# Optimization experiments

Hardware: AMD Instinct MI355X
Metric: run time of the kernel (lower is better)

Reference implementation:

```python
import jax, jax.numpy as jnp
import numpy as np

B, D, N, E = 4, 128, 16384, 65536  # batch, feature_dim, n_junctions, 2*n_lines
EPS = 1e-5  # BatchNorm eps


def setup_inputs() -> dict:
    key = jax.random.key(0)
    ks = jax.random.split(key, 8)
    s = lambda k, shape: jax.random.normal(k, shape, dtype=jnp.float32)
    return {
        "ldesc0": s(ks[0], (B, D, N)),
        "ldesc1": s(ks[1], (B, D, N)),
        "line_enc0": s(ks[2], (B, D, E)),
        "line_enc1": s(ks[3], (B, D, E)),
        "lines_junc_idx0": jax.random.randint(ks[4], (B, E), 0, N),
        "lines_junc_idx1": jax.random.randint(ks[5], (B, E), 0, N),
        # MLP([3D, 2D, D]) params: conv1x1 -> BN -> ReLU -> conv1x1
        "w1": s(ks[6], (2 * D, 3 * D)) * 0.05,
        "b1": jnp.zeros((2 * D,), jnp.float32),
        "bn_gamma": jnp.ones((2 * D,), jnp.float32),
        "bn_beta": jnp.zeros((2 * D,), jnp.float32),
        "bn_mean": jnp.zeros((2 * D,), jnp.float32),
        "bn_var": jnp.ones((2 * D,), jnp.float32),
        "w2": s(ks[7], (D, 2 * D)) * 0.05,
        "b2": jnp.zeros((D,), jnp.float32),
    }


def _mlp(x, w1, b1, g, beta, mu, var, w2, b2):
    # x: [B, 3D, E] -> [B, D, E]; BN in inference mode with running stats
    h = jnp.einsum('oi,bie->boe', w1, x) + b1[None, :, None]
    scale = g / jnp.sqrt(var + EPS)
    h = h * scale[None, :, None] + (beta - mu * scale)[None, :, None]
    h = jax.nn.relu(h)
    return jnp.einsum('oi,bie->boe', w2, h) + b2[None, :, None]


def _endpoint_update(ldesc, line_enc, idx, params):
    # gather endpoint descriptors: [B, D, E]
    line_desc = jax.vmap(lambda x, i: x[:, i])(ldesc, idx)
    b, d, e = line_desc.shape
    # swap the two endpoints of each line (flip along the size-2 axis)
    flipped = line_desc.reshape(b, d, e // 2, 2)[..., ::-1].reshape(b, d, e)
    message = jnp.concatenate([line_desc, flipped, line_enc], axis=1)  # [B, 3D, E]
    return _mlp(message, *params)


def _scatter_mean(src, idx, n):
    # src: [B, D, E], idx: [B, E] -> mean-reduced [B, D, n]; empty slots stay 0
    def one(s, i):
        sums = jax.ops.segment_sum(s.T, i, num_segments=n)                    # [n, D]
        cnt = jax.ops.segment_sum(jnp.ones(s.shape[1], s.dtype), i, num_segments=n)
        return (sums / jnp.maximum(cnt, 1.0)[:, None]).T                      # [D, n]
    return jax.vmap(one)(src, idx)


def reference(ldesc0, ldesc1, line_enc0, line_enc1, lines_junc_idx0, lines_junc_idx1,
              w1, b1, bn_gamma, bn_beta, bn_mean, bn_var, w2, b2):
    params = (w1, b1, bn_gamma, bn_beta, bn_mean, bn_var, w2, b2)
    up0 = _endpoint_update(ldesc0, line_enc0, lines_junc_idx0, params)
    up1 = _endpoint_update(ldesc1, line_enc1, lines_junc_idx1, params)
    n = ldesc0.shape[2]
    out0 = ldesc0 + _scatter_mean(up0, lines_junc_idx0, n)
    out1 = ldesc1 + _scatter_mean(up1, lines_junc_idx1, n)
    return (out0, out1)
```

## Files before the change

### kernel.cpp

```cpp
#include <hip/hip_runtime.h>
#include <hip/hip_bf16.h>
#include <stdint.h>

#define Bb 4
#define Dd 128
#define Nn 16384
#define Ee 65536
#define NTB 16

typedef __attribute__((ext_vector_type(4))) float f32x4;
typedef __attribute__((ext_vector_type(8))) short s16x8;

__device__ __forceinline__ unsigned short f2bf(float f) {
  union { float f; unsigned int u; } v; v.f = f;
  unsigned int r = v.u + 0x7fffu + ((v.u >> 16) & 1u);
  return (unsigned short)(r >> 16);
}

__device__ __forceinline__ unsigned int cvtpk(float lo, float hi) {
  unsigned int r;
  asm volatile("v_cvt_pk_bf16_f32 %0, %1, %2" : "=v"(r) : "v"(lo), "v"(hi));
  return r;
}

__global__ void prep_weights(const float* __restrict__ w1, const float* __restrict__ b1,
                             const float* __restrict__ g, const float* __restrict__ beta,
                             const float* __restrict__ mu, const float* __restrict__ var,
                             const float* __restrict__ w2,
                             unsigned short* __restrict__ W1s, unsigned short* __restrict__ W2s,
                             float* __restrict__ c1) {
  int i = blockIdx.x * 256 + threadIdx.x;
  if (i < 256 * 384) {
    int o = i / 384;
    float scale = g[o] * rsqrtf(var[o] + 1e-5f);
    W1s[i] = f2bf(w1[i] * scale);
  }
  if (i < 128 * 256) W2s[i] = f2bf(w2[i]);
  if (i < 256) {
    float scale = g[i] * rsqrtf(var[i] + 1e-5f);
    c1[i] = b1[i] * scale + beta[i] - mu[i] * scale;
  }
}

__global__ void transpose_ldesc(const float* __restrict__ l0, const float* __restrict__ l1,
                                unsigned short* __restrict__ dst, int side0) {
  __shared__ float tile[32][33];
  int z = blockIdx.z;
  int gs = side0 + (z >> 2), b = z & 3;
  const float* src = (gs ? l1 : l0) + (size_t)b * Dd * Nn;
  unsigned short* d = dst + (size_t)z * Nn * Dd;
  int n0 = blockIdx.x * 32;
  int d0 = blockIdx.y * 32;
  int tx = threadIdx.x, ty = threadIdx.y;
#pragma unroll
  for (int i = 0; i < 4; ++i)
    tile[ty + i * 8][tx] = src[(size_t)(d0 + ty + i * 8) * Nn + n0 + tx];
  __syncthreads();
#pragma unroll
  for (int i = 0; i < 4; ++i) {
    int r = ty + i * 8;
    d[(size_t)(n0 + r) * Dd + d0 + tx] = f2bf(tile[tx][r]);
  }
}

__global__ void hist_kernel(const int* __restrict__ idx0, const int* __restrict__ idx1,
                            int* __restrict__ hist) {
  int i = blockIdx.x * 256 + threadIdx.x;
  int sb = i >> 16;
  int e = i & 65535;
  const int* jx = (sb >= 4) ? idx1 : idx0;
  int n = jx[(size_t)(sb & 3) * Ee + e];
  atomicAdd(&hist[sb * Nn + n], 1);
}

__global__ __launch_bounds__(1024) void scan_kernel(const int* __restrict__ hist,
                                                    int* __restrict__ offs,
                                                    int* __restrict__ cursor) {
  __shared__ int part[1024];
  int sb = blockIdx.x, t = threadIdx.x;
  const int* h = hist + sb * Nn;
  int base = t * 16;
  int v[16];
  int local = 0;
#pragma unroll
  for (int i = 0; i < 16; ++i) { v[i] = local; local += h[base + i]; }
  part[t] = local;
  __syncthreads();
  for (int d = 1; d < 1024; d <<= 1) {
    int y = (t >= d) ? part[t - d] : 0;
    __syncthreads();
    part[t] += y;
    __syncthreads();
  }
  int excl = part[t] - local;
#pragma unroll
  for (int i = 0; i < 16; ++i) {
    int o = excl + v[i];
    offs[sb * Nn + base + i] = o;
    cursor[sb * Nn + base + i] = o;
  }
}

__global__ void fill_kernel(const int* __restrict__ idx0, const int* __restrict__ idx1,
                            int* __restrict__ cursor, int* __restrict__ elist) {
  int i = blockIdx.x * 256 + threadIdx.x;
  int sb = i >> 16;
  int e = i & 65535;
  const int* jx = (sb >= 4) ? idx1 : idx0;
  int n = jx[(size_t)(sb & 3) * Ee + e];
  int pos = atomicAdd(&cursor[sb * Nn + n], 1);
  elist[(size_t)sb * Ee + pos] = e;
}

#define STAGE_DESC(ti, buf)                                                     \
  do {                                                                          \
    int e0s_ = (tile0 + (ti)) * 64;                                             \
    unsigned char* xb_ = sm + (buf) * 32768;                                    \
    int cA_ = w * 8 + (lane >> 4);                                              \
    int cB_ = cA_ + 4;                                                          \
    int uA_ = (lane & 15) ^ (cA_ & 7);                                          \
    int uB_ = (lane & 15) ^ (cB_ & 7);                                          \
    int iA_ = jxB[e0s_ + cA_];                                                  \
    int iB_ = jxB[e0s_ + cB_];                                                  \
    __builtin_amdgcn_global_load_lds(                                           \
        (const __attribute__((address_space(1))) void*)(ldB + ((size_t)iA_) * 128 + uA_ * 8), \
        (__attribute__((address_space(3))) void*)(xb_ + (w * 8) * 256), 16, 0, 0); \
    __builtin_amdgcn_global_load_lds(                                           \
        (const __attribute__((address_space(1))) void*)(ldB + ((size_t)iB_) * 128 + uB_ * 8), \
        (__attribute__((address_space(3))) void*)(xb_ + (w * 8 + 4) * 256), 16, 0, 0); \
  } while (0)

#define ENC_LOAD(ti)                                                            \
  do {                                                                          \
    int e0s_ = (tile0 + (ti)) * 64;                                             \
    const float* es_ = enF + (size_t)(oct * 8) * Ee + e0s_ + ep * 2;            \
    _Pragma("unroll") for (int r = 0; r < 8; ++r)                               \
      ereg[r] = *(const float2*)(es_ + (size_t)r * Ee);                         \
  } while (0)

#define ENC_WRITE(buf)                                                          \
  do {                                                                          \
    unsigned char* xb_ = sm + (buf) * 32768;                                    \
    _Pragma("unroll") for (int j = 0; j < 2; ++j) {                             \
      int e_ = ep * 2 + j;                                                      \
      uint4 pk_;                                                                \
      pk_.x = cvtpk(j ? ereg[0].y : ereg[0].x, j ? ereg[1].y : ereg[1].x);      \
      pk_.y = cvtpk(j ? ereg[2].y : ereg[2].x, j ? ereg[3].y : ereg[3].x);      \
      pk_.z = cvtpk(j ? ereg[4].y : ereg[4].x, j ? ereg[5].y : ereg[5].x);      \
      pk_.w = cvtpk(j ? ereg[6].y : ereg[6].x, j ? ereg[7].y : ereg[7].x);      \
      *(uint4*)(xb_ + 16384 + e_ * 256 + ((oct ^ (e_ & 7)) << 4)) = pk_;        \
    }                                                                           \
  } while (0)

__global__ __launch_bounds__(512, 2) void fused_mlp_ws(
    const unsigned short* __restrict__ ldescT,
    const float* __restrict__ enc0, const float* __restrict__ enc1,
    const int* __restrict__ idx0, const int* __restrict__ idx1, int side0,
    const unsigned short* __restrict__ W1s, const unsigned short* __restrict__ W2s,
    const float* __restrict__ c1, const float* __restrict__ b2,
    unsigned short* __restrict__ U) {
  __shared__ __align__(16) unsigned char sm[65536];

  const int t = threadIdx.x;
  const int w = t >> 6;
  const int lane = t & 63;
  const int lr = t & 15;
  const int lk = (t & 63) >> 4;
  const int oct = t >> 5;
  const int ep = t & 31;
  const int ls = blockIdx.x >> 8;
  const int gs = side0 + ls;
  const int bB = (blockIdx.x >> 6) & 3;
  const int tile0 = (blockIdx.x & 63) * NTB;

  const int* jxB = (gs ? idx1 : idx0) + (size_t)bB * Ee;
  const unsigned short* ldB = ldescT + ((size_t)(ls * Bb + bB)) * Nn * 128;
  const float* enF = (gs ? enc1 : enc0) + (size_t)bB * Dd * Ee;
  unsigned short* UB = U + ((size_t)(ls * Bb + bB)) * Ee * 128;

  s16x8 w1f[2][12];
#pragma unroll
  for (int rt = 0; rt < 2; ++rt)
#pragma unroll
    for (int ks = 0; ks < 12; ++ks)
      w1f[rt][ks] = *(const s16x8*)&W1s[(size_t)(w * 32 + rt * 16 + lr) * 384 + ks * 32 + lk * 8];
  s16x8 w2f[8];
#pragma unroll
  for (int ks = 0; ks < 8; ++ks)
    w2f[ks] = *(const s16x8*)&W2s[(size_t)(w * 16 + lr) * 256 + ks * 32 + lk * 8];
  float c1v[2][4], b2v[4];
#pragma unroll
  for (int rt = 0; rt < 2; ++rt)
#pragma unroll
    for (int r = 0; r < 4; ++r) c1v[rt][r] = c1[w * 32 + rt * 16 + lk * 4 + r];
#pragma unroll
  for (int r = 0; r < 4; ++r) b2v[r] = b2[w * 16 + lk * 4 + r];

  float2 ereg[8];

  STAGE_DESC(0, 0);
  STAGE_DESC(1, 1);
  ENC_LOAD(0);
  asm volatile("s_waitcnt vmcnt(0)" ::: "memory");
  ENC_WRITE(0);
  ENC_LOAD(1);
  asm volatile("s_waitcnt vmcnt(0)" ::: "memory");
  ENC_WRITE(1);
  asm volatile("s_waitcnt lgkmcnt(0)" ::: "memory");
  __builtin_amdgcn_s_barrier();
  __builtin_amdgcn_sched_barrier(0);

#pragma unroll 1
  for (int i = 0; i < NTB; ++i) {
    const int p = i & 1;
    unsigned short* xb = (unsigned short*)(sm + p * 32768);
    unsigned short* hb = xb;
    const int e0c = (tile0 + i) * 64;

    f32x4 acc[2][4] = {};
    __builtin_amdgcn_s_setprio(1);
#pragma unroll
    for (int ks = 0; ks < 12; ++ks) {
      s16x8 bf[4];
#pragma unroll
      for (int ct = 0; ct < 4; ++ct) {
        int c = ct * 16 + lr;
        int off;
        if (ks < 4)      { off = c * 128 + (((ks * 4 + lk) ^ (c & 7)) * 8); }
        else if (ks < 8) { int c2 = c ^ 1; off = c2 * 128 + ((((ks - 4) * 4 + lk) ^ (c2 & 7)) * 8); }
        else             { off = 8192 + c * 128 + ((((ks - 8) * 4 + lk) ^ (c & 7)) * 8); }
        bf[ct] = *(const s16x8*)&xb[off];
      }
#pragma unroll
      for (int rt = 0; rt < 2; ++rt)
#pragma unroll
        for (int ct = 0; ct < 4; ++ct)
          acc[rt][ct] = __builtin_amdgcn_mfma_f32_16x16x32_bf16(w1f[rt][ks], bf[ct], acc[rt][ct], 0, 0, 0);
    }
    __builtin_amdgcn_s_setprio(0);
    asm volatile("s_waitcnt lgkmcnt(0)" ::: "memory");
    __builtin_amdgcn_s_barrier();
    __builtin_amdgcn_sched_barrier(0);

#pragma unroll
    for (int rt = 0; rt < 2; ++rt) {
      int rowbase = w * 32 + rt * 16 + lk * 4;
      int unitr = rowbase >> 3, inner = rowbase & 7;
#pragma unroll
      for (int ct = 0; ct < 4; ++ct) {
        int col = ct * 16 + lr;
        float v0 = fmaxf(acc[rt][ct][0] + c1v[rt][0], 0.f);
        float v1 = fmaxf(acc[rt][ct][1] + c1v[rt][1], 0.f);
        float v2 = fmaxf(acc[rt][ct][2] + c1v[rt][2], 0.f);
        float v3 = fmaxf(acc[rt][ct][3] + c1v[rt][3], 0.f);
        uint2 pk;
        pk.x = cvtpk(v0, v1);
        pk.y = cvtpk(v2, v3);
        *(uint2*)&hb[col * 256 + ((unitr ^ (col & 7)) * 8) + inner] = pk;
      }
    }

    if (i + 2 < NTB) ENC_LOAD(i + 2);

    asm volatile("s_waitcnt lgkmcnt(0)" ::: "memory");
    __builtin_amdgcn_s_barrier();
    __builtin_amdgcn_sched_barrier(0);

    f32x4 acc2[4] = {};
    __builtin_amdgcn_s_setprio(1);
#pragma unroll
    for (int ks = 0; ks < 8; ++ks) {
      s16x8 bf[4];
#pragma unroll
      for (int ct = 0; ct < 4; ++ct) {
        int c = ct * 16 + lr;
        bf[ct] = *(const s16x8*)&hb[c * 256 + (((ks * 4 + lk) ^ (c & 7)) * 8)];
      }
#pragma unroll
      for (int ct = 0; ct < 4; ++ct)
        acc2[ct] = __builtin_amdgcn_mfma_f32_16x16x32_bf16(w2f[ks], bf[ct], acc2[ct], 0, 0, 0);
    }
    __builtin_amdgcn_s_setprio(0);

#pragma unroll
    for (int ct = 0; ct < 4; ++ct) {
      int col = ct * 16 + lr;
      uint2 pk;
      pk.x = cvtpk(acc2[ct][0] + b2v[0], acc2[ct][1] + b2v[1]);
      pk.y = cvtpk(acc2[ct][2] + b2v[2], acc2[ct][3] + b2v[3]);
      *(uint2*)&UB[(((size_t)(e0c + col)) << 7) + w * 16 + lk * 4] = pk;
    }

    asm volatile("s_waitcnt lgkmcnt(0)" ::: "memory");
    __builtin_amdgcn_s_barrier();
    __builtin_amdgcn_sched_barrier(0);

    if (i + 2 < NTB) {
      asm volatile("s_waitcnt vmcnt(0)" ::: "memory");
      ENC_WRITE(p);
      STAGE_DESC(i + 2, p);
    }

    if (i + 1 < NTB) {
      if (i + 2 >= NTB)
        asm volatile("s_waitcnt vmcnt(0)" ::: "memory");
      asm volatile("s_waitcnt lgkmcnt(0)" ::: "memory");
      __builtin_amdgcn_s_barrier();
      __builtin_amdgcn_sched_barrier(0);
    }
  }
}

__global__ __launch_bounds__(256) void scatter_finalize(
    const unsigned short* __restrict__ U, const int* __restrict__ elist,
    const int* __restrict__ offs, const float* __restrict__ l0,
    const float* __restrict__ l1, float* __restrict__ out, int side0) {
  __shared__ float lsum[64][129];
  const int ls = blockIdx.z;
  const int gs = side0 + ls;
  const int b = blockIdx.y;
  const int n0 = blockIdx.x * 64;
  const int t = threadIdx.x;
  const int w = t >> 6, lane = t & 63;
  const unsigned int* Uu = (const unsigned int*)(U + ((size_t)(ls * Bb + b)) * Ee * 128);
  const int* elist_s = elist + ((size_t)(gs * Bb + b)) * Ee;
  const int* offs_s = offs + ((size_t)(gs * Bb + b)) * Nn;
  const float* l = (gs ? l1 : l0) + (size_t)b * Dd * Nn;
  float* o = out + ((size_t)(gs * Bb + b)) * Dd * Nn;

#pragma unroll 1
  for (int q = 0; q < 16; ++q) {
    int jj = w * 16 + q;
    int n = n0 + jj;
    int s = offs_s[n];
    int e_end = (n == Nn - 1) ? Ee : offs_s[n + 1];
    float s0 = 0.f, s1 = 0.f;
    for (int k = s; k < e_end; ++k) {
      int e = elist_s[k];
      unsigned int p = Uu[(((size_t)e) << 6) + lane];
      union { unsigned int u; float f; } lo, hi;
      lo.u = p << 16;
      hi.u = p & 0xffff0000u;
      s0 += lo.f;
      s1 += hi.f;
    }
    float inv = (e_end > s) ? 1.0f / (float)(e_end - s) : 0.0f;
    lsum[jj][lane * 2] = s0 * inv;
    lsum[jj][lane * 2 + 1] = s1 * inv;
  }
  __syncthreads();

  int nloc = t & 63;
  int dbase = (t >> 6) * 32;
#pragma unroll
  for (int i = 0; i < 32; ++i) {
    int d = dbase + i;
    size_t off2 = (size_t)d * Nn + n0 + nloc;
    o[off2] = l[off2] + lsum[nloc][d];
  }
}

extern "C" void kernel_launch(void* const* d_in, const int* in_sizes, int n_in,
                              void* d_out, int out_size, void* d_ws, size_t ws_size,
                              hipStream_t stream) {
  const float* ldesc0 = (const float*)d_in[0];
  const float* ldesc1 = (const float*)d_in[1];
  const float* enc0   = (const float*)d_in[2];
  const float* enc1   = (const float*)d_in[3];
  const int*   idx0   = (const int*)d_in[4];
  const int*   idx1   = (const int*)d_in[5];
  const float* w1     = (const float*)d_in[6];
  const float* b1     = (const float*)d_in[7];
  const float* g      = (const float*)d_in[8];
  const float* beta   = (const float*)d_in[9];
  const float* mu     = (const float*)d_in[10];
  const float* var    = (const float*)d_in[11];
  const float* w2     = (const float*)d_in[12];
  const float* b2     = (const float*)d_in[13];
  float* out = (float*)d_out;

  char* ws = (char*)d_ws;
  size_t off = 0;
  unsigned short* W1s = (unsigned short*)(ws + off); off += 256 * 384 * 2;
  unsigned short* W2s = (unsigned short*)(ws + off); off += 128 * 256 * 2;
  float* c1   = (float*)(ws + off); off += 256 * 4;
  int* hist   = (int*)(ws + off); off += (size_t)8 * Nn * 4;
  int* offs   = (int*)(ws + off); off += (size_t)8 * Nn * 4;
  int* cursor = (int*)(ws + off); off += (size_t)8 * Nn * 4;
  int* elist  = (int*)(ws + off); off += (size_t)8 * Ee * 4;
  size_t small_end = off;

  const size_t tside = (size_t)Bb * Nn * Dd * 2;
  const size_t bigside = (size_t)Bb * Ee * Dd * 2;
  size_t need_full = small_end + 2 * tside + 2 * bigside;
  const bool full = (ws_size >= need_full);
  const int sides_buf = full ? 2 : 1;

  unsigned short* t = (unsigned short*)(ws + off); off += tside * sides_buf;
  unsigned short* U = (unsigned short*)(ws + off); off += bigside * sides_buf;

  hipMemsetAsync(hist, 0, (size_t)8 * Nn * 4, stream);
  prep_weights<<<384, 256, 0, stream>>>(w1, b1, g, beta, mu, var, w2, W1s, W2s, c1);
  hist_kernel<<<2048, 256, 0, stream>>>(idx0, idx1, hist);
  scan_kernel<<<8, 1024, 0, stream>>>(hist, offs, cursor);
  fill_kernel<<<2048, 256, 0, stream>>>(idx0, idx1, cursor, elist);

  if (full) {
    transpose_ldesc<<<dim3(Nn / 32, Dd / 32, 8), dim3(32, 8), 0, stream>>>(
        ldesc0, ldesc1, t, 0);
    fused_mlp_ws<<<512, 512, 0, stream>>>(t, enc0, enc1, idx0, idx1, 0,
                                          W1s, W2s, c1, b2, U);
    scatter_finalize<<<dim3(Nn / 64, Bb, 2), 256, 0, stream>>>(
        U, elist, offs, ldesc0, ldesc1, out, 0);
  } else {
    for (int side = 0; side < 2; ++side) {
      transpose_ldesc<<<dim3(Nn / 32, Dd / 32, 4), dim3(32, 8), 0, stream>>>(
          ldesc0, ldesc1, t, side);
      fused_mlp_ws<<<256, 512, 0, stream>>>(t, enc0, enc1, idx0, idx1, side,
                                            W1s, W2s, c1, b2, U);
      scatter_finalize<<<dim3(Nn / 64, Bb, 1), 256, 0, stream>>>(
          U, elist, offs, ldesc0, ldesc1, out, side);
    }
  }
}
```

Before: 460.5 us.

## Write MLP outputs in junction-sorted order and deepen encoder prefetch pipeline

fill_kernel now stores each edge's sorted position (perm), and the fused MLP writes each edge's output row directly at that position. The scatter kernel can then read U contiguously per junction without the elist indirection. The MLP kernel also gets a separate 32KB LDS buffer for the hidden activations, so one barrier per tile can be dropped and the encoder loads can run three tiles ahead with partial vmcnt waits. In exchange, LDS per block grows to 96KB, which may lower occupancy below the 2 blocks per CU that the launch bounds target, and the U stores become scattered rows.

```diff
diff --git a/kernel.cpp b/kernel.cpp
--- a/kernel.cpp
+++ b/kernel.cpp
@@ -102,14 +102,14 @@
 }
 
 __global__ void fill_kernel(const int* __restrict__ idx0, const int* __restrict__ idx1,
-                            int* __restrict__ cursor, int* __restrict__ elist) {
+                            int* __restrict__ cursor, int* __restrict__ perm) {
   int i = blockIdx.x * 256 + threadIdx.x;
   int sb = i >> 16;
   int e = i & 65535;
   const int* jx = (sb >= 4) ? idx1 : idx0;
   int n = jx[(size_t)(sb & 3) * Ee + e];
   int pos = atomicAdd(&cursor[sb * Nn + n], 1);
-  elist[(size_t)sb * Ee + pos] = e;
+  perm[(size_t)sb * Ee + e] = pos;
 }
 
 #define STAGE_DESC(ti, buf)                                                     \
@@ -156,10 +156,11 @@
     const unsigned short* __restrict__ ldescT,
     const float* __restrict__ enc0, const float* __restrict__ enc1,
     const int* __restrict__ idx0, const int* __restrict__ idx1, int side0,
+    const int* __restrict__ perm,
     const unsigned short* __restrict__ W1s, const unsigned short* __restrict__ W2s,
     const float* __restrict__ c1, const float* __restrict__ b2,
     unsigned short* __restrict__ U) {
-  __shared__ __align__(16) unsigned char sm[65536];
+  __shared__ __align__(16) unsigned char sm[98304];
 
   const int t = threadIdx.x;
   const int w = t >> 6;
@@ -174,6 +175,7 @@
   const int tile0 = (blockIdx.x & 63) * NTB;
 
   const int* jxB = (gs ? idx1 : idx0) + (size_t)bB * Ee;
+  const int* permB = perm + ((size_t)(gs * Bb + bB)) * Ee;
   const unsigned short* ldB = ldescT + ((size_t)(ls * Bb + bB)) * Nn * 128;
   const float* enF = (gs ? enc1 : enc0) + (size_t)bB * Dd * Ee;
   unsigned short* UB = U + ((size_t)(ls * Bb + bB)) * Ee * 128;
@@ -197,6 +199,7 @@
   for (int r = 0; r < 4; ++r) b2v[r] = b2[w * 16 + lk * 4 + r];
 
   float2 ereg[8];
+  unsigned short* hb = (unsigned short*)(sm + 65536);
 
   STAGE_DESC(0, 0);
   STAGE_DESC(1, 1);
@@ -206,6 +209,7 @@
   ENC_LOAD(1);
   asm volatile("s_waitcnt vmcnt(0)" ::: "memory");
   ENC_WRITE(1);
+  if (2 < NTB) ENC_LOAD(2);
   asm volatile("s_waitcnt lgkmcnt(0)" ::: "memory");
   __builtin_amdgcn_s_barrier();
   __builtin_amdgcn_sched_barrier(0);
@@ -213,9 +217,12 @@
 #pragma unroll 1
   for (int i = 0; i < NTB; ++i) {
     const int p = i & 1;
-    unsigned short* xb = (unsigned short*)(sm + p * 32768);
-    unsigned short* hb = xb;
+    const unsigned short* xb = (const unsigned short*)(sm + p * 32768);
     const int e0c = (tile0 + i) * 64;
+
+    int prow[4];
+#pragma unroll
+    for (int ct = 0; ct < 4; ++ct) prow[ct] = permB[e0c + ct * 16 + lr];
 
     f32x4 acc[2][4] = {};
     __builtin_amdgcn_s_setprio(1);
@@ -238,9 +245,6 @@
           acc[rt][ct] = __builtin_amdgcn_mfma_f32_16x16x32_bf16(w1f[rt][ks], bf[ct], acc[rt][ct], 0, 0, 0);
     }
     __builtin_amdgcn_s_setprio(0);
-    asm volatile("s_waitcnt lgkmcnt(0)" ::: "memory");
-    __builtin_amdgcn_s_barrier();
-    __builtin_amdgcn_sched_barrier(0);
 
 #pragma unroll
     for (int rt = 0; rt < 2; ++rt) {
@@ -259,12 +263,20 @@
         *(uint2*)&hb[col * 256 + ((unitr ^ (col & 7)) * 8) + inner] = pk;
       }
     }
-
-    if (i + 2 < NTB) ENC_LOAD(i + 2);
-
     asm volatile("s_waitcnt lgkmcnt(0)" ::: "memory");
     __builtin_amdgcn_s_barrier();
     __builtin_amdgcn_sched_barrier(0);
+
+    if (i == 0) {
+      asm volatile("s_waitcnt vmcnt(4)" ::: "memory");
+    } else {
+      asm volatile("s_waitcnt vmcnt(8)" ::: "memory");
+    }
+    if (i + 2 < NTB) {
+      ENC_WRITE(p);
+      STAGE_DESC(i + 2, p);
+    }
+    if (i + 3 < NTB) ENC_LOAD(i + 3);
 
     f32x4 acc2[4] = {};
     __builtin_amdgcn_s_setprio(1);
@@ -284,26 +296,13 @@
 
 #pragma unroll
     for (int ct = 0; ct < 4; ++ct) {
-      int col = ct * 16 + lr;
       uint2 pk;
       pk.x = cvtpk(acc2[ct][0] + b2v[0], acc2[ct][1] + b2v[1]);
       pk.y = cvtpk(acc2[ct][2] + b2v[2], acc2[ct][3] + b2v[3]);
-      *(uint2*)&UB[(((size_t)(e0c + col)) << 7) + w * 16 + lk * 4] = pk;
-    }
-
-    asm volatile("s_waitcnt lgkmcnt(0)" ::: "memory");
-    __builtin_amdgcn_s_barrier();
-    __builtin_amdgcn_sched_barrier(0);
-
-    if (i + 2 < NTB) {
-      asm volatile("s_waitcnt vmcnt(0)" ::: "memory");
-      ENC_WRITE(p);
-      STAGE_DESC(i + 2, p);
+      *(uint2*)&UB[(((size_t)prow[ct]) << 7) + w * 16 + lk * 4] = pk;
     }
 
     if (i + 1 < NTB) {
-      if (i + 2 >= NTB)
-        asm volatile("s_waitcnt vmcnt(0)" ::: "memory");
       asm volatile("s_waitcnt lgkmcnt(0)" ::: "memory");
       __builtin_amdgcn_s_barrier();
       __builtin_amdgcn_sched_barrier(0);
@@ -312,7 +311,7 @@
 }
 
 __global__ __launch_bounds__(256) void scatter_finalize(
-    const unsigned short* __restrict__ U, const int* __restrict__ elist,
+    const unsigned short* __restrict__ U,
     const int* __restrict__ offs, const float* __restrict__ l0,
     const float* __restrict__ l1, float* __restrict__ out, int side0) {
   __shared__ float lsum[64][129];
@@ -323,7 +322,6 @@
   const int t = threadIdx.x;
   const int w = t >> 6, lane = t & 63;
   const unsigned int* Uu = (const unsigned int*)(U + ((size_t)(ls * Bb + b)) * Ee * 128);
-  const int* elist_s = elist + ((size_t)(gs * Bb + b)) * Ee;
   const int* offs_s = offs + ((size_t)(gs * Bb + b)) * Nn;
   const float* l = (gs ? l1 : l0) + (size_t)b * Dd * Nn;
   float* o = out + ((size_t)(gs * Bb + b)) * Dd * Nn;
@@ -336,8 +334,7 @@
     int e_end = (n == Nn - 1) ? Ee : offs_s[n + 1];
     float s0 = 0.f, s1 = 0.f;
     for (int k = s; k < e_end; ++k) {
-      int e = elist_s[k];
-      unsigned int p = Uu[(((size_t)e) << 6) + lane];
+      unsigned int p = Uu[(((size_t)k) << 6) + lane];
       union { unsigned int u; float f; } lo, hi;
       lo.u = p << 16;
       hi.u = p & 0xffff0000u;
@@ -387,7 +384,7 @@
   int* hist   = (int*)(ws + off); off += (size_t)8 * Nn * 4;
   int* offs   = (int*)(ws + off); off += (size_t)8 * Nn * 4;
   int* cursor = (int*)(ws + off); off += (size_t)8 * Nn * 4;
-  int* elist  = (int*)(ws + off); off += (size_t)8 * Ee * 4;
+  int* perm   = (int*)(ws + off); off += (size_t)8 * Ee * 4;
   size_t small_end = off;
 
   const size_t tside = (size_t)Bb * Nn * Dd * 2;
@@ -403,23 +400,23 @@
   prep_weights<<<384, 256, 0, stream>>>(w1, b1, g, beta, mu, var, w2, W1s, W2s, c1);
   hist_kernel<<<2048, 256, 0, stream>>>(idx0, idx1, hist);
   scan_kernel<<<8, 1024, 0, stream>>>(hist, offs, cursor);
-  fill_kernel<<<2048, 256, 0, stream>>>(idx0, idx1, cursor, elist);
+  fill_kernel<<<2048, 256, 0, stream>>>(idx0, idx1, cursor, perm);
 
   if (full) {
     transpose_ldesc<<<dim3(Nn / 32, Dd / 32, 8), dim3(32, 8), 0, stream>>>(
         ldesc0, ldesc1, t, 0);
-    fused_mlp_ws<<<512, 512, 0, stream>>>(t, enc0, enc1, idx0, idx1, 0,
+    fused_mlp_ws<<<512, 512, 0, stream>>>(t, enc0, enc1, idx0, idx1, 0, perm,
                                           W1s, W2s, c1, b2, U);
     scatter_finalize<<<dim3(Nn / 64, Bb, 2), 256, 0, stream>>>(
-        U, elist, offs, ldesc0, ldesc1, out, 0);
+        U, offs, ldesc0, ldesc1, out, 0);
   } else {
     for (int side = 0; side < 2; ++side) {
       transpose_ldesc<<<dim3(Nn / 32, Dd / 32, 4), dim3(32, 8), 0, stream>>>(
           ldesc0, ldesc1, t, side);
-      fused_mlp_ws<<<256, 512, 0, stream>>>(t, enc0, enc1, idx0, idx1, side,
+      fused_mlp_ws<<<256, 512, 0, stream>>>(t, enc0, enc1, idx0, idx1, side, perm,
                                             W1s, W2s, c1, b2, U);
       scatter_finalize<<<dim3(Nn / 64, Bb, 1), 256, 0, stream>>>(
-          U, elist, offs, ldesc0, ldesc1, out, side);
-    }
-  }
-}
+          U, offs, ldesc0, ldesc1, out, side);
+    }
+  }
+}
```

Measured after the change: 384.5 us. -16.5%, faster.
